# Kernel tuning notes

Measured on AMD Instinct MI355X. Metric: run time of the kernel, lower is better.

Reference implementation:

```python
import jax, jax.numpy as jnp
import numpy as np

L = 5           # num_layer
D = 128         # emb_dim
N = 100_000     # num nodes
E = 1_600_000   # num edges
EDGE_F = 7      # raw edge feature dim
BN_EPS = 1e-5


def batchnorm(z, gamma, beta):
    # BatchNorm1d in training-style normalization: biased batch mean/var over axis 0
    mu = z.mean(axis=0)
    var = z.var(axis=0)
    return gamma * (z - mu) * jax.lax.rsqrt(var + BN_EPS) + beta


def setup_inputs() -> dict:
    key = jax.random.key(0)
    ks = jax.random.split(key, 16)
    s = 0.05
    return {
        "x": jnp.zeros((N,), jnp.int32),                               # Embedding(1, D) indices
        "edge_index": jax.random.randint(ks[0], (2, E), 0, N, jnp.int32),
        "edge_attr": jax.random.normal(ks[1], (E, EDGE_F), jnp.float32),
        "node_emb": jax.random.normal(ks[2], (1, D), jnp.float32) * s,
        "We": jax.random.normal(ks[3], (L, EDGE_F, D), jnp.float32) * s,   # edge_encoder weight
        "be": jax.random.normal(ks[4], (L, D), jnp.float32) * s,
        "eps": jnp.zeros((L,), jnp.float32),                               # GIN eps, init 0
        "W1": jax.random.normal(ks[5], (L, D, 2 * D), jnp.float32) * s,
        "b1": jax.random.normal(ks[6], (L, 2 * D), jnp.float32) * s,
        "g1": jnp.ones((L, 2 * D), jnp.float32),                           # mlp inner BN gamma
        "bt1": jnp.zeros((L, 2 * D), jnp.float32),                         # mlp inner BN beta
        "W2": jax.random.normal(ks[7], (L, 2 * D, D), jnp.float32) * s,
        "b2": jax.random.normal(ks[8], (L, D), jnp.float32) * s,
        "gbn": jnp.ones((L, D), jnp.float32),                              # outer BN gamma
        "bbn": jnp.zeros((L, D), jnp.float32),                             # outer BN beta
    }


def reference(x, edge_index, edge_attr, node_emb, We, be, eps, W1, b1, g1, bt1, W2, b2, gbn, bbn):
    # node encoder (Embedding with vocab=1)
    h = node_emb[x]                       # [N, D]
    src, dst = edge_index[0], edge_index[1]
    for l in range(L):
        # edge embedding + GIN message: relu(x_j + edge_emb), scatter-add at dst
        ee = edge_attr @ We[l] + be[l]                       # [E, D]
        msg = jax.nn.relu(h[src] + ee)                       # gather + add + relu
        agg = jax.ops.segment_sum(msg, dst, num_segments=N)  # scatter-add
        out = (1.0 + eps[l]) * h + agg                       # [N, D]
        # mlp: Linear(D,2D) -> BN -> ReLU -> Linear(2D,D)
        z = batchnorm(out @ W1[l] + b1[l], g1[l], bt1[l])
        z = jax.nn.relu(z) @ W2[l] + b2[l]
        # outer BatchNorm; dropout is identity in eval mode
        h = batchnorm(z, gbn[l], bbn[l])
        if l < L - 1:
            h = jax.nn.relu(h)
    return h
```

## Files before the change

### kernel.cpp

```cpp
#include <hip/hip_runtime.h>
#include <cstddef>

#define NN 100000
#define NE 1600000
#define D 128
#define D2 256
#define EF 7
#define NL 5
#define BN_EPS 1e-5f
#define GW 12500

typedef unsigned short ushort_t;
typedef __attribute__((ext_vector_type(8))) _Float16 f16x8;
typedef __attribute__((ext_vector_type(2))) _Float16 h2v;
typedef __attribute__((ext_vector_type(4))) float f32x4;

__device__ __forceinline__ void atomAddF(float* p, float v) { unsafeAtomicAdd(p, v); }

__device__ __forceinline__ ushort_t f2h(float f) {
    return __builtin_bit_cast(ushort_t, (_Float16)f);
}
__device__ __forceinline__ unsigned pk2h(float lo, float hi) {
    return (unsigned)f2h(lo) | ((unsigned)f2h(hi) << 16);
}
__device__ __forceinline__ float h2f(unsigned u16) {
    return (float)__builtin_bit_cast(_Float16, (ushort_t)(u16 & 0xFFFFu));
}
__device__ __forceinline__ h2v u2h2(unsigned u) { return __builtin_bit_cast(h2v, u); }

__global__ __launch_bounds__(256)
void hist_kernel(const int* __restrict__ ei, int* __restrict__ counts)
{
    const int e = blockIdx.x * 256 + threadIdx.x;
    if (e < NE) atomicAdd(&counts[ei[NE + e]], 1);
}

__global__ __launch_bounds__(1024)
void scan_kernel(const int* __restrict__ counts, int* __restrict__ offs)
{
    __shared__ int ssum[1024];
    const int t = threadIdx.x;
    const int per = (NN + 1023) / 1024;
    const int base = t * per;
    int local = 0;
    for (int j = 0; j < per; ++j) {
        const int i = base + j;
        if (i < NN) local += counts[i];
    }
    ssum[t] = local;
    __syncthreads();
    for (int off = 1; off < 1024; off <<= 1) {
        int v = 0;
        if (t >= off) v = ssum[t - off];
        __syncthreads();
        ssum[t] += v;
        __syncthreads();
    }
    int run = ssum[t] - local;
    for (int j = 0; j < per; ++j) {
        const int i = base + j;
        if (i < NN) { offs[i] = run; run += counts[i]; }
    }
    if (t == 1023) offs[NN] = NE;
}

__global__ __launch_bounds__(256)
void scatter_kernel(const int* __restrict__ ei, const float* __restrict__ ea,
                    int* __restrict__ offmut, int* __restrict__ sSrc,
                    ushort_t* __restrict__ eaH)
{
    const int e = blockIdx.x * 256 + threadIdx.x;
    if (e < NE) {
        const int dst = ei[NE + e];
        const int pos = atomicAdd(&offmut[dst], 1);
        sSrc[pos] = ei[e];
        const float* eap = &ea[(size_t)e * EF];
        const unsigned o0 = pk2h(eap[0], eap[1]);
        const unsigned o1 = pk2h(eap[2], eap[3]);
        const unsigned o2 = pk2h(eap[4], eap[5]);
        const unsigned o3 = pk2h(eap[6], 0.f);
        *(uint4*)&eaH[(size_t)pos * 8] = make_uint4(o0, o1, o2, o3);
    }
}

__global__ __launch_bounds__(256)
void wconv_kernel(const float* __restrict__ W1, const float* __restrict__ W2,
                  ushort_t* __restrict__ W1t, ushort_t* __restrict__ W2t)
{
    const int idx = blockIdx.x * 256 + threadIdx.x;
    const int per = D * D2;
    if (idx < NL * per) {
        const int l = idx / per, r = idx % per;
        const int k1 = r / D2, n1 = r % D2;
        W1t[(size_t)l * per + n1 * D + k1] = f2h(W1[idx]);
        const int k2 = r / D, n2 = r % D;
        W2t[(size_t)l * per + n2 * D2 + k2] = f2h(W2[idx]);
    }
}

template<int L0>
__global__ __launch_bounds__(256)
void gather_kernel(const int* __restrict__ offs, const int* __restrict__ sSrc,
                   const ushort_t* __restrict__ eaH,
                   const float* __restrict__ We, const float* __restrict__ be,
                   const ushort_t* __restrict__ hAct, const float* __restrict__ h0,
                   const float* __restrict__ epsp,
                   ushort_t* __restrict__ xinH, float* __restrict__ xsum)
{
    __shared__ __align__(16) float sCS[4][D];
    const int lane = threadIdx.x & 63;
    const int w = threadIdx.x >> 6;
    const int wid = blockIdx.x * 4 + w;

    const float2* We2 = (const float2*)We;
    const unsigned* hU = (const unsigned*)hAct;
    unsigned* xU = (unsigned*)xinH;
    h2v wP[EF];
    #pragma unroll
    for (int k = 0; k < EF; ++k) {
        const float2 wf = We2[k * 64 + lane];
        wP[k] = (h2v){(_Float16)wf.x, (_Float16)wf.y};
    }
    h2v beP;
    {
        const float2 bf = ((const float2*)be)[lane];
        beP = (h2v){(_Float16)bf.x, (_Float16)bf.y};
    }
    float2 h0v = {0.f, 0.f};
    h2v h0P = (h2v){(_Float16)0.f, (_Float16)0.f};
    if (L0) {
        h0v = ((const float2*)h0)[lane];
        h0P = (h2v){(_Float16)h0v.x, (_Float16)h0v.y};
    }
    const float epsv = 1.0f + *epsp;
    const h2v zz = (h2v){(_Float16)0.f, (_Float16)0.f};

    int p4[8], e4[8];
    #pragma unroll
    for (int i = 0; i < 8; ++i) {
        const int n = wid + i * GW;
        p4[i] = __builtin_amdgcn_readfirstlane(offs[n]);
        e4[i] = __builtin_amdgcn_readfirstlane(offs[n + 1]);
    }
    int mx = 0;
    #pragma unroll
    for (int i = 0; i < 8; ++i) mx = max(mx, e4[i] - p4[i]);

    float2 acc[8];
    #pragma unroll
    for (int i = 0; i < 8; ++i) acc[i] = (float2){0.f, 0.f};

    for (int j = 0; j < mx; ++j) {
        unsigned hwd[8];
        uint4 ev4[8];
        bool on[8];
        #pragma unroll
        for (int i = 0; i < 8; ++i) {
            on[i] = p4[i] < e4[i];
            if (on[i]) {
                ev4[i] = *(const uint4*)&eaH[(size_t)p4[i] * 8];
                if (!L0) {
                    const int src = sSrc[p4[i]];
                    hwd[i] = hU[(src << 6) + lane];
                }
            }
        }
        #pragma unroll
        for (int i = 0; i < 8; ++i) {
            if (on[i]) {
                const h2v e01 = u2h2(ev4[i].x);
                const h2v e23 = u2h2(ev4[i].y);
                const h2v e45 = u2h2(ev4[i].z);
                const h2v e6x = u2h2(ev4[i].w);
                h2v m = beP;
                m = __builtin_elementwise_fma(__builtin_shufflevector(e01, e01, 0, 0), wP[0], m);
                m = __builtin_elementwise_fma(__builtin_shufflevector(e01, e01, 1, 1), wP[1], m);
                m = __builtin_elementwise_fma(__builtin_shufflevector(e23, e23, 0, 0), wP[2], m);
                m = __builtin_elementwise_fma(__builtin_shufflevector(e23, e23, 1, 1), wP[3], m);
                m = __builtin_elementwise_fma(__builtin_shufflevector(e45, e45, 0, 0), wP[4], m);
                m = __builtin_elementwise_fma(__builtin_shufflevector(e45, e45, 1, 1), wP[5], m);
                m = __builtin_elementwise_fma(__builtin_shufflevector(e6x, e6x, 0, 0), wP[6], m);
                const h2v hh = L0 ? h0P : u2h2(hwd[i]);
                const h2v r = __builtin_elementwise_max(m + hh, zz);
                acc[i].x += (float)r.x;
                acc[i].y += (float)r.y;
                ++p4[i];
            }
        }
    }

    float2 cs = {0.f, 0.f};
    #pragma unroll
    for (int i = 0; i < 8; ++i) {
        const int n = wid + i * GW;
        float2 hs;
        if (L0) hs = h0v;
        else {
            const unsigned hv = hU[(n << 6) + lane];
            hs.x = h2f(hv); hs.y = h2f(hv >> 16);
        }
        float2 a = acc[i];
        a.x = fmaf(epsv, hs.x, a.x);
        a.y = fmaf(epsv, hs.y, a.y);
        cs.x += a.x; cs.y += a.y;
        xU[(n << 6) + lane] = pk2h(a.x, a.y);
    }
    sCS[w][2 * lane] = cs.x;
    sCS[w][2 * lane + 1] = cs.y;
    __syncthreads();
    if (threadIdx.x < D) {
        atomAddF(&xsum[threadIdx.x],
                 sCS[0][threadIdx.x] + sCS[1][threadIdx.x] +
                 sCS[2][threadIdx.x] + sCS[3][threadIdx.x]);
    }
}

__global__ __launch_bounds__(256, 2)
void mm1_kernel(const ushort_t* __restrict__ xinH, const float* __restrict__ xsum,
                const ushort_t* __restrict__ W1t,
                ushort_t* __restrict__ z1H, float* __restrict__ stats)
{
    __shared__ __align__(16) ushort_t sA[64 * 128];
    __shared__ __align__(16) float sM[D];
    const int t = threadIdx.x;
    if (t < D) sM[t] = xsum[t] * (1.0f / (float)NN);
    const int i0 = blockIdx.x * 64;
    const int lane = t & 63, w = t >> 6;
    const int nb = w * 64;

    f16x8 bfr[4][4];
    #pragma unroll
    for (int nt = 0; nt < 4; ++nt)
        #pragma unroll
        for (int ks = 0; ks < 4; ++ks) {
            const int n = nb + nt * 16 + (lane & 15);
            const int k = ks * 32 + (lane >> 4) * 8;
            bfr[nt][ks] = *(const f16x8*)&W1t[n * D + k];
        }
    __syncthreads();

    #pragma unroll
    for (int p = 0; p < 4; ++p) {
        const int linear = p * 256 + t;
        const int row = linear >> 4, ch = linear & 15;
        const int gi = i0 + row;
        unsigned oo[4] = {0, 0, 0, 0};
        if (gi < NN) {
            const uint4 v = *(const uint4*)&xinH[(size_t)gi * D + ch * 8];
            const unsigned uu[4] = {v.x, v.y, v.z, v.w};
            #pragma unroll
            for (int j2 = 0; j2 < 4; ++j2) {
                const int c0 = ch * 8 + j2 * 2;
                oo[j2] = pk2h(h2f(uu[j2]) - sM[c0], h2f(uu[j2] >> 16) - sM[c0 + 1]);
            }
        }
        unsigned boff = (unsigned)(row * 256 + ch * 16);
        boff ^= (unsigned)((row & 7) << 4);
        *(uint4*)((char*)sA + boff) = make_uint4(oo[0], oo[1], oo[2], oo[3]);
    }
    __syncthreads();

    f32x4 acc[4][4];
    #pragma unroll
    for (int a = 0; a < 4; ++a)
        #pragma unroll
        for (int b = 0; b < 4; ++b) acc[a][b] = (f32x4){0.f, 0.f, 0.f, 0.f};

    #pragma unroll
    for (int mt = 0; mt < 4; ++mt) {
        f16x8 af[4];
        #pragma unroll
        for (int ks = 0; ks < 4; ++ks) {
            const int row = mt * 16 + (lane & 15);
            unsigned boff = (unsigned)(row * 256 + ks * 64 + (lane >> 4) * 16);
            boff ^= (unsigned)((row & 7) << 4);
            af[ks] = *(const f16x8*)((const char*)sA + boff);
        }
        #pragma unroll
        for (int nt = 0; nt < 4; ++nt)
            #pragma unroll
            for (int ks = 0; ks < 4; ++ks)
                acc[mt][nt] = __builtin_amdgcn_mfma_f32_16x16x32_f16(af[ks], bfr[nt][ks], acc[mt][nt], 0, 0, 0);
    }

    float s[4], q[4];
    #pragma unroll
    for (int nt = 0; nt < 4; ++nt) { s[nt] = 0.f; q[nt] = 0.f; }
    #pragma unroll
    for (int nt = 0; nt < 4; ++nt) {
        const int n = nb + nt * 16 + (lane & 15);
        #pragma unroll
        for (int mt = 0; mt < 4; ++mt)
            #pragma unroll
            for (int r = 0; r < 4; ++r) {
                const int i = i0 + mt * 16 + (lane >> 4) * 4 + r;
                if (i < NN) {
                    const float v = acc[mt][nt][r];
                    s[nt] += v; q[nt] = fmaf(v, v, q[nt]);
                    z1H[(size_t)i * D2 + n] = f2h(v);
                }
            }
    }
    #pragma unroll
    for (int nt = 0; nt < 4; ++nt) {
        s[nt] += __shfl_xor(s[nt], 16, 64); s[nt] += __shfl_xor(s[nt], 32, 64);
        q[nt] += __shfl_xor(q[nt], 16, 64); q[nt] += __shfl_xor(q[nt], 32, 64);
    }
    if (lane < 16) {
        #pragma unroll
        for (int nt = 0; nt < 4; ++nt) {
            const int n = nb + nt * 16 + lane;
            atomAddF(&stats[n], s[nt]);
            atomAddF(&stats[D2 + n], q[nt]);
        }
    }
}

__global__ __launch_bounds__(256, 2)
void mm2_kernel(const ushort_t* __restrict__ z1H, const float* __restrict__ stats1,
                const float* __restrict__ g1, const float* __restrict__ bt1,
                const ushort_t* __restrict__ W2t,
                ushort_t* __restrict__ z2H, float* __restrict__ stats2)
{
    __shared__ __align__(16) ushort_t sA[64 * 256];
    __shared__ __align__(16) float sAff[2 * D2];
    __shared__ __align__(16) float sYm[D2];
    const int t = threadIdx.x;
    {
        const float inv = 1.0f / (float)NN;
        const float mu = stats1[t] * inv;
        const float var = fmaf(-mu, mu, stats1[D2 + t] * inv);
        const float a = g1[t] * rsqrtf(var + BN_EPS);
        sAff[t] = a;
        sAff[D2 + t] = fmaf(-a, mu, bt1[t]);
        const float m0 = bt1[t];
        const float sg = fabsf(g1[t]);
        float ym;
        if (sg > 1e-20f) {
            const float r = m0 / sg;
            const float Ph = 0.5f * (1.0f + erff(r * 0.70710678f));
            const float ph = 0.39894228f * expf(-0.5f * r * r);
            ym = m0 * Ph + sg * ph;
        } else {
            ym = fmaxf(m0, 0.f);
        }
        sYm[t] = ym;
    }
    const int i0 = blockIdx.x * 64;
    const int lane = t & 63, w = t >> 6;
    const int nb = w * 32;

    f16x8 bfr[2][8];
    #pragma unroll
    for (int nt = 0; nt < 2; ++nt)
        #pragma unroll
        for (int ks = 0; ks < 8; ++ks) {
            const int n = nb + nt * 16 + (lane & 15);
            const int k = ks * 32 + (lane >> 4) * 8;
            bfr[nt][ks] = *(const f16x8*)&W2t[n * D2 + k];
        }
    __syncthreads();

    #pragma unroll
    for (int p = 0; p < 8; ++p) {
        const int linear = p * 256 + t;
        const int row = linear >> 5, ch = linear & 31;
        const int gi = i0 + row;
        unsigned oo[4] = {0, 0, 0, 0};
        if (gi < NN) {
            const uint4 v = *(const uint4*)&z1H[(size_t)gi * D2 + ch * 8];
            const unsigned uu[4] = {v.x, v.y, v.z, v.w};
            #pragma unroll
            for (int j2 = 0; j2 < 4; ++j2) {
                const int c0 = ch * 8 + j2 * 2;
                float lo = h2f(uu[j2]);
                float hi = h2f(uu[j2] >> 16);
                lo = fmaxf(fmaf(sAff[c0], lo, sAff[D2 + c0]), 0.f) - sYm[c0];
                hi = fmaxf(fmaf(sAff[c0 + 1], hi, sAff[D2 + c0 + 1]), 0.f) - sYm[c0 + 1];
                oo[j2] = pk2h(lo, hi);
            }
        }
        unsigned boff = (unsigned)(row * 512 + ch * 16);
        boff ^= (unsigned)((row & 7) << 4);
        *(uint4*)((char*)sA + boff) = make_uint4(oo[0], oo[1], oo[2], oo[3]);
    }
    __syncthreads();

    f32x4 acc[4][2];
    #pragma unroll
    for (int a = 0; a < 4; ++a)
        #pragma unroll
        for (int b = 0; b < 2; ++b) acc[a][b] = (f32x4){0.f, 0.f, 0.f, 0.f};

    #pragma unroll
    for (int mt = 0; mt < 4; ++mt) {
        f16x8 af[8];
        #pragma unroll
        for (int ks = 0; ks < 8; ++ks) {
            const int row = mt * 16 + (lane & 15);
            unsigned boff = (unsigned)(row * 512 + ks * 64 + (lane >> 4) * 16);
            boff ^= (unsigned)((row & 7) << 4);
            af[ks] = *(const f16x8*)((const char*)sA + boff);
        }
        #pragma unroll
        for (int nt = 0; nt < 2; ++nt)
            #pragma unroll
            for (int ks = 0; ks < 8; ++ks)
                acc[mt][nt] = __builtin_amdgcn_mfma_f32_16x16x32_f16(af[ks], bfr[nt][ks], acc[mt][nt], 0, 0, 0);
    }

    float s[2], q[2];
    #pragma unroll
    for (int nt = 0; nt < 2; ++nt) { s[nt] = 0.f; q[nt] = 0.f; }
    #pragma unroll
    for (int nt = 0; nt < 2; ++nt) {
        const int n = nb + nt * 16 + (lane & 15);
        #pragma unroll
        for (int mt = 0; mt < 4; ++mt)
            #pragma unroll
            for (int r = 0; r < 4; ++r) {
                const int i = i0 + mt * 16 + (lane >> 4) * 4 + r;
                if (i < NN) {
                    const float v = acc[mt][nt][r];
                    s[nt] += v; q[nt] = fmaf(v, v, q[nt]);
                    z2H[(size_t)i * D + n] = f2h(v);
                }
            }
    }
    #pragma unroll
    for (int nt = 0; nt < 2; ++nt) {
        s[nt] += __shfl_xor(s[nt], 16, 64); s[nt] += __shfl_xor(s[nt], 32, 64);
        q[nt] += __shfl_xor(q[nt], 16, 64); q[nt] += __shfl_xor(q[nt], 32, 64);
    }
    if (lane < 16) {
        #pragma unroll
        for (int nt = 0; nt < 2; ++nt) {
            const int n = nb + nt * 16 + lane;
            atomAddF(&stats2[n], s[nt]);
            atomAddF(&stats2[D + n], q[nt]);
        }
    }
}

template<int HALF>
__global__ __launch_bounds__(256)
void act_kernel(const ushort_t* __restrict__ z2H, const float* __restrict__ stats2,
                const float* __restrict__ g, const float* __restrict__ bt,
                void* __restrict__ dstv)
{
    __shared__ float sA[D], sC[D];
    const int t = threadIdx.x;
    if (t < D) {
        const float inv = 1.0f / (float)NN;
        const float mu = stats2[t] * inv;
        const float var = fmaf(-mu, mu, stats2[D + t] * inv);
        const float a = g[t] * rsqrtf(var + BN_EPS);
        sA[t] = a;
        sC[t] = fmaf(-a, mu, bt[t]);
    }
    __syncthreads();
    const int idx = blockIdx.x * 256 + t;
    if (idx < NN * D / 4) {
        const int d0 = (idx * 4) & (D - 1);
        const uint2 v = *(const uint2*)&z2H[(size_t)idx * 4];
        float4 o;
        o.x = fmaf(sA[d0 + 0], h2f(v.x),       sC[d0 + 0]);
        o.y = fmaf(sA[d0 + 1], h2f(v.x >> 16), sC[d0 + 1]);
        o.z = fmaf(sA[d0 + 2], h2f(v.y),       sC[d0 + 2]);
        o.w = fmaf(sA[d0 + 3], h2f(v.y >> 16), sC[d0 + 3]);
        if (HALF) {
            o.x = fmaxf(o.x, 0.f); o.y = fmaxf(o.y, 0.f);
            o.z = fmaxf(o.z, 0.f); o.w = fmaxf(o.w, 0.f);
            uint2 pkd;
            pkd.x = pk2h(o.x, o.y);
            pkd.y = pk2h(o.z, o.w);
            *((uint2*)dstv + idx) = pkd;
        } else {
            *((float4*)dstv + idx) = o;
        }
    }
}

extern "C" void kernel_launch(void* const* d_in, const int* in_sizes, int n_in,
                              void* d_out, int out_size, void* d_ws, size_t ws_size,
                              hipStream_t stream)
{
    (void)in_sizes; (void)n_in; (void)out_size; (void)ws_size;
    const int*   ei       = (const int*)d_in[1];
    const float* ea       = (const float*)d_in[2];
    const float* node_emb = (const float*)d_in[3];
    const float* We       = (const float*)d_in[4];
    const float* be       = (const float*)d_in[5];
    const float* eps      = (const float*)d_in[6];
    const float* W1       = (const float*)d_in[7];
    const float* g1       = (const float*)d_in[9];
    const float* bt1      = (const float*)d_in[10];
    const float* W2       = (const float*)d_in[11];
    const float* gbn      = (const float*)d_in[13];
    const float* bbn      = (const float*)d_in[14];
    float* out = (float*)d_out;

    char* base = (char*)d_ws;
    size_t off = 0;
    auto alloc = [&](size_t bytes) -> void* {
        void* p = base + off;
        off = (off + bytes + 255) & ~(size_t)255;
        return p;
    };
    ushort_t* tmpH   = (ushort_t*)alloc((size_t)NN * D * 2);
    ushort_t* z1H    = (ushort_t*)alloc((size_t)NN * D2 * 2);
    ushort_t* hAct   = (ushort_t*)alloc((size_t)NN * D * 2);
    ushort_t* W1t    = (ushort_t*)alloc((size_t)NL * D * D2 * 2);
    ushort_t* W2t    = (ushort_t*)alloc((size_t)NL * D * D2 * 2);
    float*    red    = (float*)alloc(896 * sizeof(float));
    float*    stats1 = red;
    float*    stats2 = red + 512;
    float*    xsum   = red + 768;
    int*      counts = (int*)alloc((NN + 1) * sizeof(int));
    int*      offs   = (int*)alloc((NN + 1) * sizeof(int));
    int*      offmut = (int*)alloc(NN * sizeof(int));
    int*      sSrc   = (int*)alloc((size_t)NE * sizeof(int));
    ushort_t* eaH    = (ushort_t*)alloc((size_t)NE * 8 * 2);

    hipMemsetAsync(counts, 0, (NN + 1) * sizeof(int), stream);
    hist_kernel<<<(NE + 255) / 256, 256, 0, stream>>>(ei, counts);
    scan_kernel<<<1, 1024, 0, stream>>>(counts, offs);
    hipMemcpyAsync(offmut, offs, NN * sizeof(int), hipMemcpyDeviceToDevice, stream);
    scatter_kernel<<<(NE + 255) / 256, 256, 0, stream>>>(ei, ea, offmut, sSrc, eaH);
    wconv_kernel<<<(NL * D * D2 + 255) / 256, 256, 0, stream>>>(W1, W2, W1t, W2t);

    for (int l = 0; l < NL; ++l) {
        hipMemsetAsync(red, 0, 896 * sizeof(float), stream);
        if (l == 0) {
            gather_kernel<1><<<GW / 4, 256, 0, stream>>>(offs, sSrc, eaH,
                                                         We + l * EF * D, be + l * D,
                                                         hAct, node_emb, eps + l, tmpH, xsum);
        } else {
            gather_kernel<0><<<GW / 4, 256, 0, stream>>>(offs, sSrc, eaH,
                                                         We + l * EF * D, be + l * D,
                                                         hAct, node_emb, eps + l, tmpH, xsum);
        }
        mm1_kernel<<<(NN + 63) / 64, 256, 0, stream>>>(tmpH, xsum, W1t + (size_t)l * D * D2,
                                                       z1H, stats1);
        mm2_kernel<<<(NN + 63) / 64, 256, 0, stream>>>(z1H, stats1, g1 + l * D2, bt1 + l * D2,
                                                       W2t + (size_t)l * D * D2,
                                                       tmpH, stats2);
        if (l < NL - 1) {
            act_kernel<1><<<(NN * D / 4 + 255) / 256, 256, 0, stream>>>(
                tmpH, stats2, gbn + l * D, bbn + l * D, hAct);
        } else {
            act_kernel<0><<<(NN * D / 4 + 255) / 256, 256, 0, stream>>>(
                tmpH, stats2, gbn + l * D, bbn + l * D, out);
        }
    }
}
```

Baseline: 1.778 ms.

## Replace single-block prefix scan with three-phase multi-block scan

```diff
diff --git a/kernel.cpp b/kernel.cpp
--- a/kernel.cpp
+++ b/kernel.cpp
@@ -9,6 +9,7 @@
 #define NL 5
 #define BN_EPS 1e-5f
 #define GW 12500
+#define SCAN_NB ((NN + 1023) / 1024)
 
 typedef unsigned short ushort_t;
 typedef __attribute__((ext_vector_type(8))) _Float16 f16x8;
@@ -35,33 +36,74 @@
     if (e < NE) atomicAdd(&counts[ei[NE + e]], 1);
 }
 
-__global__ __launch_bounds__(1024)
-void scan_kernel(const int* __restrict__ counts, int* __restrict__ offs)
-{
-    __shared__ int ssum[1024];
+__global__ __launch_bounds__(256)
+void scanA_kernel(const int* __restrict__ counts, int* __restrict__ bsum)
+{
+    __shared__ int sred[256];
     const int t = threadIdx.x;
-    const int per = (NN + 1023) / 1024;
-    const int base = t * per;
-    int local = 0;
-    for (int j = 0; j < per; ++j) {
+    const int base = blockIdx.x * 1024 + t * 4;
+    int s = 0;
+    #pragma unroll
+    for (int j = 0; j < 4; ++j) { const int i = base + j; if (i < NN) s += counts[i]; }
+    sred[t] = s;
+    __syncthreads();
+    for (int off = 128; off > 0; off >>= 1) {
+        if (t < off) sred[t] += sred[t + off];
+        __syncthreads();
+    }
+    if (t == 0) bsum[blockIdx.x] = sred[0];
+}
+
+__global__ __launch_bounds__(128)
+void scanB_kernel(const int* __restrict__ bsum, int* __restrict__ bbase,
+                  int* __restrict__ offs)
+{
+    __shared__ int ss[128];
+    const int t = threadIdx.x;
+    const int v = (t < SCAN_NB) ? bsum[t] : 0;
+    ss[t] = v;
+    __syncthreads();
+    for (int off = 1; off < 128; off <<= 1) {
+        int u = 0;
+        if (t >= off) u = ss[t - off];
+        __syncthreads();
+        ss[t] += u;
+        __syncthreads();
+    }
+    if (t < SCAN_NB) bbase[t] = ss[t] - v;
+    if (t == 0) offs[NN] = NE;
+}
+
+__global__ __launch_bounds__(256)
+void scanC_kernel(const int* __restrict__ counts, const int* __restrict__ bbase,
+                  int* __restrict__ offs)
+{
+    __shared__ int sts[256];
+    const int t = threadIdx.x;
+    const int base = blockIdx.x * 1024 + t * 4;
+    int c[4];
+    int s = 0;
+    #pragma unroll
+    for (int j = 0; j < 4; ++j) {
         const int i = base + j;
-        if (i < NN) local += counts[i];
-    }
-    ssum[t] = local;
-    __syncthreads();
-    for (int off = 1; off < 1024; off <<= 1) {
-        int v = 0;
-        if (t >= off) v = ssum[t - off];
+        c[j] = (i < NN) ? counts[i] : 0;
+        s += c[j];
+    }
+    sts[t] = s;
+    __syncthreads();
+    for (int off = 1; off < 256; off <<= 1) {
+        int u = 0;
+        if (t >= off) u = sts[t - off];
         __syncthreads();
-        ssum[t] += v;
+        sts[t] += u;
         __syncthreads();
     }
-    int run = ssum[t] - local;
-    for (int j = 0; j < per; ++j) {
+    int run = bbase[blockIdx.x] + sts[t] - s;
+    #pragma unroll
+    for (int j = 0; j < 4; ++j) {
         const int i = base + j;
-        if (i < NN) { offs[i] = run; run += counts[i]; }
-    }
-    if (t == 1023) offs[NN] = NE;
+        if (i < NN) { offs[i] = run; run += c[j]; }
+    }
 }
 
 __global__ __launch_bounds__(256)
@@ -519,12 +561,16 @@
     int*      counts = (int*)alloc((NN + 1) * sizeof(int));
     int*      offs   = (int*)alloc((NN + 1) * sizeof(int));
     int*      offmut = (int*)alloc(NN * sizeof(int));
+    int*      bsum   = (int*)alloc(SCAN_NB * sizeof(int));
+    int*      bbase  = (int*)alloc(SCAN_NB * sizeof(int));
     int*      sSrc   = (int*)alloc((size_t)NE * sizeof(int));
     ushort_t* eaH    = (ushort_t*)alloc((size_t)NE * 8 * 2);
 
     hipMemsetAsync(counts, 0, (NN + 1) * sizeof(int), stream);
     hist_kernel<<<(NE + 255) / 256, 256, 0, stream>>>(ei, counts);
-    scan_kernel<<<1, 1024, 0, stream>>>(counts, offs);
+    scanA_kernel<<<SCAN_NB, 256, 0, stream>>>(counts, bsum);
+    scanB_kernel<<<1, 128, 0, stream>>>(bsum, bbase, offs);
+    scanC_kernel<<<SCAN_NB, 256, 0, stream>>>(counts, bbase, offs);
     hipMemcpyAsync(offmut, offs, NN * sizeof(int), hipMemcpyDeviceToDevice, stream);
     scatter_kernel<<<(NE + 255) / 256, 256, 0, stream>>>(ei, ea, offmut, sSrc, eaH);
     wconv_kernel<<<(NL * D * D2 + 255) / 256, 256, 0, stream>>>(W1, W2, W1t, W2t);
```

Result: faster. 1.606 ms (-9.7%).
